# Kernel optimization log

Measured on AMD Instinct MI355X. Metric: run time of the kernel, lower is better.

## Reference

```python
import jax, jax.numpy as jnp
import numpy as np

N_NODES = 50000
N_EDGES = 800000
F_IN = 64
H = 128
N_CLASSES = 10
NUM_GRAPHS = 512


def setup_inputs() -> dict:
    key = jax.random.key(0)
    ks = jax.random.split(key, 16)
    x = jax.random.normal(ks[0], (N_NODES, F_IN), dtype=jnp.float32)
    edge_index = jax.random.randint(ks[1], (2, N_EDGES), 0, N_NODES, dtype=jnp.int64)
    batch = jnp.sort(jax.random.randint(ks[2], (N_NODES,), 0, NUM_GRAPHS, dtype=jnp.int64))

    def lin(k, fi, fo):
        kw, kb = jax.random.split(k)
        s = 1.0 / np.sqrt(fi)
        return (jax.random.uniform(kw, (fi, fo), jnp.float32, -s, s),
                jax.random.uniform(kb, (fo,), jnp.float32, -s, s))

    W0, b0 = lin(ks[3], F_IN, H)
    W1, b1 = lin(ks[4], H, H)
    W2, b2 = lin(ks[5], H, H)
    mW0, mb0 = lin(ks[6], H, H)
    mW1, mb1 = lin(ks[7], H, H)
    mW2, mb2 = lin(ks[8], H, N_CLASSES)
    return {"x": x, "edge_index": edge_index, "batch": batch,
            "W0": W0, "b0": b0, "W1": W1, "b1": b1, "W2": W2, "b2": b2,
            "mW0": mW0, "mb0": mb0, "mW1": mW1, "mb1": mb1, "mW2": mW2, "mb2": mb2}


def reference(x, edge_index, batch, W0, b0, W1, b1, W2, b2, mW0, mb0, mW1, mb1, mW2, mb2):
    N = x.shape[0]
    loop = jnp.arange(N, dtype=edge_index.dtype)
    src = jnp.concatenate([edge_index[0], loop])  # add self-loops (PyG GCNConv)
    dst = jnp.concatenate([edge_index[1], loop])
    deg = jax.ops.segment_sum(jnp.ones_like(src, jnp.float32), dst, num_segments=N)
    dinv = jnp.where(deg > 0, deg ** -0.5, 0.0)
    norm = dinv[src] * dinv[dst]  # [E+N]

    def gcn(h, W, b):
        h = h @ W                                   # [N, H]
        msg = h[src] * norm[:, None]                # gather [E+N, H]
        return jax.ops.segment_sum(msg, dst, num_segments=N) + b

    h = jax.nn.relu(gcn(x, W0, b0))
    h = jax.nn.relu(gcn(h, W1, b1))
    h = jax.nn.relu(gcn(h, W2, b2))
    g = jax.ops.segment_sum(h, batch, num_segments=NUM_GRAPHS)  # global_add_pool
    g = jax.nn.relu(g @ mW0 + mb0)
    g = jax.nn.relu(g @ mW1 + mb1)
    return g @ mW2 + mb2  # [NUM_GRAPHS, N_CLASSES]
```

## Files before the change

kernel.cpp:

```cpp
#include <hip/hip_runtime.h>
#include <hip/hip_bf16.h>
#include <stdint.h>

#define N_NODES   50000
#define N_EDGES   800000
#define F_IN      64
#define HID       128
#define N_CLASSES 10
#define NUM_GRAPHS 512

#define NBUCK 128
#define BW    391
#define S1B   400
#define CHUNK 2000
#define MCNT  (NBUCK * S1B)

typedef unsigned int uint32;
typedef __attribute__((ext_vector_type(8))) short bf16x8;
typedef __attribute__((ext_vector_type(4))) float f32x4;

__device__ __forceinline__ float bl(uint32 w) { return __uint_as_float(w << 16); }
__device__ __forceinline__ float bh(uint32 w) { return __uint_as_float(w & 0xffff0000u); }
__device__ __forceinline__ uint32 packbf(float a, float b) {
    uint32 ua = __float_as_uint(a), ub = __float_as_uint(b);
    ua = (ua + 0x7fffu + ((ua >> 16) & 1u)) >> 16;
    ub = (ub + 0x7fffu + ((ub >> 16) & 1u)) >> 16;
    return ua | (ub << 16);
}
__device__ __forceinline__ unsigned short packbf1(float a) {
    uint32 ua = __float_as_uint(a);
    return (unsigned short)((ua + 0x7fffu + ((ua >> 16) & 1u)) >> 16);
}

__global__ __launch_bounds__(256) void prep_kernel(const float4* __restrict__ x, uint2* __restrict__ xb,
                                                   const float* __restrict__ W0, unsigned short* __restrict__ W0t,
                                                   const float* __restrict__ W1, unsigned short* __restrict__ W1t,
                                                   const float* __restrict__ W2, unsigned short* __restrict__ W2t) {
    int i = blockIdx.x * 256 + threadIdx.x;
    if (i < N_NODES * F_IN / 4) {
        float4 v = x[i];
        xb[i] = make_uint2(packbf(v.x, v.y), packbf(v.z, v.w));
    }
    if (i < 64 * 128) {
        int k = i >> 7, j = i & 127;
        W0t[j * (64 + 8) + k] = packbf1(W0[i]);
    }
    int i2 = i - 64 * 128;
    if (i2 >= 0 && i2 < 128 * 128) {
        int k = i2 >> 7, j = i2 & 127;
        W1t[j * (128 + 8) + k] = packbf1(W1[i2]);
        W2t[j * (128 + 8) + k] = packbf1(W2[i2]);
    }
}

__global__ __launch_bounds__(256) void bhist_kernel(const int* __restrict__ dst,
                                                    int* __restrict__ bcnt, int E) {
    __shared__ int cnt[NBUCK];
    int t = threadIdx.x, blk = blockIdx.x;
    if (t < NBUCK) cnt[t] = 0;
    __syncthreads();
    int base = blk * CHUNK;
    for (int i = t; i < CHUNK; i += 256) {
        int e = base + i;
        if (e < E) atomicAdd(&cnt[(uint32)dst[e] / BW], 1);
    }
    __syncthreads();
    if (t < NBUCK) bcnt[t * S1B + blk] = cnt[t];
}

__global__ __launch_bounds__(256) void scanA_kernel(const int* __restrict__ in,
                                                    int* __restrict__ incl,
                                                    int* __restrict__ bsum, int M) {
    __shared__ int s[256];
    int t = threadIdx.x;
    int i = blockIdx.x * 256 + t;
    int v = (i < M) ? in[i] : 0;
    s[t] = v;
    __syncthreads();
    #pragma unroll
    for (int d = 1; d < 256; d <<= 1) {
        int a = (t >= d) ? s[t - d] : 0;
        __syncthreads();
        s[t] += a;
        __syncthreads();
    }
    if (i < M) incl[i] = s[t];
    if (t == 255) bsum[blockIdx.x] = s[255];
}

__global__ __launch_bounds__(256) void scanB_kernel(int* __restrict__ bsum, int NB) {
    __shared__ int s[256];
    int t = threadIdx.x;
    int v = (t < NB) ? bsum[t] : 0;
    s[t] = v;
    __syncthreads();
    #pragma unroll
    for (int d = 1; d < 256; d <<= 1) {
        int a = (t >= d) ? s[t - d] : 0;
        __syncthreads();
        s[t] += a;
        __syncthreads();
    }
    if (t < NB) bsum[t] = s[t] - v;
}

__global__ __launch_bounds__(256) void bscatter_kernel(const int* __restrict__ src,
                                                       const int* __restrict__ dst,
                                                       const int* __restrict__ incl,
                                                       const int* __restrict__ bsum,
                                                       int2* __restrict__ ebuf, int E) {
    __shared__ int cnt[NBUCK];
    __shared__ int cur[NBUCK];
    int t = threadIdx.x, blk = blockIdx.x;
    if (t < NBUCK) cnt[t] = 0;
    __syncthreads();
    int base = blk * CHUNK;
    for (int i = t; i < CHUNK; i += 256) {
        int e = base + i;
        if (e < E) atomicAdd(&cnt[(uint32)dst[e] / BW], 1);
    }
    __syncthreads();
    if (t < NBUCK) {
        int idx = t * S1B + blk;
        cur[t] = bsum[idx >> 8] + incl[idx] - cnt[t];
    }
    __syncthreads();
    for (int i = t; i < CHUNK; i += 256) {
        int e = base + i;
        if (e < E) {
            int d = dst[e];
            int slot = atomicAdd(&cur[(uint32)d / BW], 1);
            ebuf[slot] = make_int2(src[e], d);
        }
    }
}

__global__ __launch_bounds__(256) void bfinal_kernel(const int2* __restrict__ ebuf,
                                                     const int* __restrict__ bcnt,
                                                     const int* __restrict__ incl,
                                                     const int* __restrict__ bsum,
                                                     int* __restrict__ rowptr,
                                                     float* __restrict__ dinv,
                                                     int2* __restrict__ meta, int E, int N) {
    __shared__ int cnt[392];
    __shared__ int startv[400];
    __shared__ int segt[16];
    int t = threadIdx.x, b = blockIdx.x;

    int bs, be;
    {
        int idx = b * S1B;
        bs = bsum[idx >> 8] + incl[idx] - bcnt[idx];
        if (b + 1 >= NBUCK) be = E;
        else {
            int idx1 = (b + 1) * S1B;
            be = bsum[idx1 >> 8] + incl[idx1] - bcnt[idx1];
        }
    }

    for (int i = t; i < 392; i += 256) cnt[i] = 0;
    __syncthreads();
    for (int i = bs + t; i < be; i += 256) {
        int d = ebuf[i].y;
        atomicAdd(&cnt[d - b * BW], 1);
    }
    __syncthreads();

    if (t < 16) {
        int run = 0;
        #pragma unroll
        for (int k = 0; k < 25; k++) {
            int idx = t * 25 + k;
            int c = (idx < 391) ? cnt[idx] : 0;
            startv[idx] = run;
            run += c;
        }
        segt[t] = run;
    }
    __syncthreads();
    if (t == 0) {
        int run = 0;
        #pragma unroll
        for (int j = 0; j < 16; j++) { int s = segt[j]; segt[j] = run; run += s; }
    }
    __syncthreads();
    for (int l = t; l < 391; l += 256) startv[l] += segt[l / 25] + bs;
    __syncthreads();

    int locN = N - b * BW; if (locN > BW) locN = BW;
    for (int l = t; l < locN; l += 256) {
        int g = b * BW + l;
        rowptr[g + 1] = startv[l] + cnt[l];
        dinv[g] = rsqrtf((float)(cnt[l] + 1));
    }
    if (b == 0 && t == 0) rowptr[0] = 0;
    __syncthreads();

    for (int i = bs + t; i < be; i += 256) {
        int2 sd = ebuf[i];
        int slot = atomicAdd(&startv[sd.y - b * BW], 1);
        meta[slot] = sd;
    }
}

__global__ __launch_bounds__(256) void norm_kernel(int2* __restrict__ meta,
                                                   const float* __restrict__ dinv, int E) {
    int i = blockIdx.x * 256 + threadIdx.x;
    if (i < E) {
        int2 m = meta[i];
        meta[i] = make_int2(m.x, __float_as_int(dinv[m.x] * dinv[m.y]));
    }
}

__global__ __launch_bounds__(256) void spmm128_kernel(const int* __restrict__ rowptr,
                                                      const int2* __restrict__ meta,
                                                      const float* __restrict__ dinv,
                                                      const unsigned short* __restrict__ Hin,
                                                      unsigned short* __restrict__ Hout, int N) {
    int wave = threadIdx.x >> 6;
    int lane = threadIdx.x & 63;
    int node = blockIdx.x * 4 + wave;
    if (node >= N) return;
    int q   = lane >> 4;
    int sub = lane & 15;

    const uint4* Hv = (const uint4*)Hin;
    float di = dinv[node];
    float sn = di * di;

    float acc[8];
    if (q == 0) {
        uint4 s = Hv[(size_t)node * 16 + sub];
        acc[0] = sn * bl(s.x); acc[1] = sn * bh(s.x);
        acc[2] = sn * bl(s.y); acc[3] = sn * bh(s.y);
        acc[4] = sn * bl(s.z); acc[5] = sn * bh(s.z);
        acc[6] = sn * bl(s.w); acc[7] = sn * bh(s.w);
    } else {
        #pragma unroll
        for (int v = 0; v < 8; v++) acc[v] = 0.f;
    }

    int e0 = rowptr[node];
    int e1 = rowptr[node + 1];
    for (int e = e0; e < e1; e += 8) {
        int i0 = e + q;
        int i1 = e + 4 + q;
        int2 m0 = (i0 < e1) ? meta[i0] : make_int2(0, 0);
        int2 m1 = (i1 < e1) ? meta[i1] : make_int2(0, 0);
        float n0 = __int_as_float(m0.y);
        float n1 = __int_as_float(m1.y);
        uint4 r0 = Hv[(size_t)m0.x * 16 + sub];
        uint4 r1 = Hv[(size_t)m1.x * 16 + sub];
        acc[0] = fmaf(n0, bl(r0.x), acc[0]); acc[1] = fmaf(n0, bh(r0.x), acc[1]);
        acc[2] = fmaf(n0, bl(r0.y), acc[2]); acc[3] = fmaf(n0, bh(r0.y), acc[3]);
        acc[4] = fmaf(n0, bl(r0.z), acc[4]); acc[5] = fmaf(n0, bh(r0.z), acc[5]);
        acc[6] = fmaf(n0, bl(r0.w), acc[6]); acc[7] = fmaf(n0, bh(r0.w), acc[7]);
        acc[0] = fmaf(n1, bl(r1.x), acc[0]); acc[1] = fmaf(n1, bh(r1.x), acc[1]);
        acc[2] = fmaf(n1, bl(r1.y), acc[2]); acc[3] = fmaf(n1, bh(r1.y), acc[3]);
        acc[4] = fmaf(n1, bl(r1.z), acc[4]); acc[5] = fmaf(n1, bh(r1.z), acc[5]);
        acc[6] = fmaf(n1, bl(r1.w), acc[6]); acc[7] = fmaf(n1, bh(r1.w), acc[7]);
    }

    #pragma unroll
    for (int v = 0; v < 8; v++) {
        acc[v] += __shfl_xor(acc[v], 16);
        acc[v] += __shfl_xor(acc[v], 32);
    }

    if (q == 0) {
        uint4 o;
        o.x = packbf(acc[0], acc[1]);
        o.y = packbf(acc[2], acc[3]);
        o.z = packbf(acc[4], acc[5]);
        o.w = packbf(acc[6], acc[7]);
        ((uint4*)Hout)[(size_t)node * 16 + sub] = o;
    }
}

__global__ __launch_bounds__(256) void spmm64_kernel(const int* __restrict__ rowptr,
                                                     const int2* __restrict__ meta,
                                                     const float* __restrict__ dinv,
                                                     const unsigned short* __restrict__ Hin,
                                                     unsigned short* __restrict__ Hout, int N) {
    int wave = threadIdx.x >> 6;
    int lane = threadIdx.x & 63;
    int node = blockIdx.x * 4 + wave;
    if (node >= N) return;
    int oct = lane >> 3;
    int sub = lane & 7;

    const uint4* Hv = (const uint4*)Hin;
    float di = dinv[node];
    float sn = di * di;

    float acc[8];
    if (oct == 0) {
        uint4 s = Hv[(size_t)node * 8 + sub];
        acc[0] = sn * bl(s.x); acc[1] = sn * bh(s.x);
        acc[2] = sn * bl(s.y); acc[3] = sn * bh(s.y);
        acc[4] = sn * bl(s.z); acc[5] = sn * bh(s.z);
        acc[6] = sn * bl(s.w); acc[7] = sn * bh(s.w);
    } else {
        #pragma unroll
        for (int v = 0; v < 8; v++) acc[v] = 0.f;
    }

    int e0 = rowptr[node];
    int e1 = rowptr[node + 1];
    for (int e = e0; e < e1; e += 16) {
        int i0 = e + oct;
        int i1 = e + 8 + oct;
        int2 m0 = (i0 < e1) ? meta[i0] : make_int2(0, 0);
        int2 m1 = (i1 < e1) ? meta[i1] : make_int2(0, 0);
        float n0 = __int_as_float(m0.y);
        float n1 = __int_as_float(m1.y);
        uint4 r0 = Hv[(size_t)m0.x * 8 + sub];
        uint4 r1 = Hv[(size_t)m1.x * 8 + sub];
        acc[0] = fmaf(n0, bl(r0.x), acc[0]); acc[1] = fmaf(n0, bh(r0.x), acc[1]);
        acc[2] = fmaf(n0, bl(r0.y), acc[2]); acc[3] = fmaf(n0, bh(r0.y), acc[3]);
        acc[4] = fmaf(n0, bl(r0.z), acc[4]); acc[5] = fmaf(n0, bh(r0.z), acc[5]);
        acc[6] = fmaf(n0, bl(r0.w), acc[6]); acc[7] = fmaf(n0, bh(r0.w), acc[7]);
        acc[0] = fmaf(n1, bl(r1.x), acc[0]); acc[1] = fmaf(n1, bh(r1.x), acc[1]);
        acc[2] = fmaf(n1, bl(r1.y), acc[2]); acc[3] = fmaf(n1, bh(r1.y), acc[3]);
        acc[4] = fmaf(n1, bl(r1.z), acc[4]); acc[5] = fmaf(n1, bh(r1.z), acc[5]);
        acc[6] = fmaf(n1, bl(r1.w), acc[6]); acc[7] = fmaf(n1, bh(r1.w), acc[7]);
    }

    #pragma unroll
    for (int v = 0; v < 8; v++) {
        acc[v] += __shfl_xor(acc[v], 8);
        acc[v] += __shfl_xor(acc[v], 16);
        acc[v] += __shfl_xor(acc[v], 32);
    }

    if (oct == 0) {
        uint4 o;
        o.x = packbf(acc[0], acc[1]);
        o.y = packbf(acc[2], acc[3]);
        o.z = packbf(acc[4], acc[5]);
        o.w = packbf(acc[6], acc[7]);
        ((uint4*)Hout)[(size_t)node * 8 + sub] = o;
    }
}

template <int K>
__global__ __launch_bounds__(256) void gemm_mfma_kernel(const unsigned short* __restrict__ A,
                                                        const unsigned short* __restrict__ Wt,
                                                        const float* __restrict__ bias,
                                                        unsigned short* __restrict__ out,
                                                        int N) {
    constexpr int KP = K + 8;
    __shared__ unsigned short Wl[128 * KP];

    int t = threadIdx.x;
    constexpr int TOT = 128 * KP * 2 / 16;
    #pragma unroll
    for (int i = 0; i < (TOT + 255) / 256; i++) {
        int idx = i * 256 + t;
        if (idx < TOT) ((uint4*)Wl)[idx] = ((const uint4*)Wt)[idx];
    }
    __syncthreads();

    int wave = t >> 6;
    int lane = t & 63;
    int rowBase = blockIdx.x * 128 + wave * 32;
    int r0 = rowBase + (lane & 15);
    int r1 = r0 + 16;
    if (r0 >= N) r0 = N - 1;
    if (r1 >= N) r1 = N - 1;
    int kchunk = lane >> 4;
    int colSub = lane & 15;

    f32x4 acc0[8], acc1[8];
    #pragma unroll
    for (int i = 0; i < 8; i++) { acc0[i] = (f32x4)0.0f; acc1[i] = (f32x4)0.0f; }

    #pragma unroll
    for (int s = 0; s < K / 32; s++) {
        bf16x8 a0 = *(const bf16x8*)(A + (size_t)r0 * K + s * 32 + kchunk * 8);
        bf16x8 a1 = *(const bf16x8*)(A + (size_t)r1 * K + s * 32 + kchunk * 8);
        #pragma unroll
        for (int tl = 0; tl < 8; tl++) {
            bf16x8 b = *(const bf16x8*)(Wl + (tl * 16 + colSub) * KP + s * 32 + kchunk * 8);
            acc0[tl] = __builtin_amdgcn_mfma_f32_16x16x32_bf16(a0, b, acc0[tl], 0, 0, 0);
            acc1[tl] = __builtin_amdgcn_mfma_f32_16x16x32_bf16(a1, b, acc1[tl], 0, 0, 0);
        }
    }

    int rowOff = (lane >> 4) * 4;
    #pragma unroll
    for (int tl = 0; tl < 8; tl++) {
        int col = tl * 16 + colSub;
        float bv = bias[col];
        #pragma unroll
        for (int r = 0; r < 4; r++) {
            int rowA = rowBase + rowOff + r;
            int rowB = rowA + 16;
            if (rowA < N) {
                float v = fmaxf(acc0[tl][r] + bv, 0.f);
                out[(size_t)rowA * 128 + col] = packbf1(v);
            }
            if (rowB < N) {
                float v = fmaxf(acc1[tl][r] + bv, 0.f);
                out[(size_t)rowB * 128 + col] = packbf1(v);
            }
        }
    }
}

__device__ __forceinline__ int lowerb(const int* a, int n, int v) {
    int lo = 0, hi = n;
    while (lo < hi) {
        int m = (lo + hi) >> 1;
        if (a[m] < v) lo = m + 1; else hi = m;
    }
    return lo;
}

__global__ __launch_bounds__(256) void pool_mlp_kernel(const unsigned short* __restrict__ H,
                                                       const int* __restrict__ batch,
                                                       const float* __restrict__ mW0, const float* __restrict__ mb0,
                                                       const float* __restrict__ mW1, const float* __restrict__ mb1,
                                                       const float* __restrict__ mW2, const float* __restrict__ mb2,
                                                       float* __restrict__ out, int N) {
    int b = blockIdx.x;
    int t = threadIdx.x;
    int jw = t & 63;
    int g  = t >> 6;
    int lo = lowerb(batch, N, b);
    int hi = lowerb(batch, N, b + 1);

    const uint32* Hu = (const uint32*)H;
    float f0 = 0.f, f1 = 0.f;
    for (int n = lo + g; n < hi; n += 4) {
        uint32 v = Hu[(size_t)n * 64 + jw];
        f0 += bl(v);
        f1 += bh(v);
    }

    __shared__ float part[4][HID];
    __shared__ float l0[HID];
    __shared__ float l1[HID];
    part[g][jw * 2 + 0] = f0;
    part[g][jw * 2 + 1] = f1;
    __syncthreads();
    if (t < 128) l0[t] = part[0][t] + part[1][t] + part[2][t] + part[3][t];
    __syncthreads();

    if (t < 128) {
        int j = t;
        float a0 = mb0[j], a1 = 0.f, a2 = 0.f, a3 = 0.f;
        #pragma unroll 4
        for (int k = 0; k < HID; k += 4) {
            a0 = fmaf(l0[k + 0], mW0[(k + 0) * HID + j], a0);
            a1 = fmaf(l0[k + 1], mW0[(k + 1) * HID + j], a1);
            a2 = fmaf(l0[k + 2], mW0[(k + 2) * HID + j], a2);
            a3 = fmaf(l0[k + 3], mW0[(k + 3) * HID + j], a3);
        }
        l1[j] = fmaxf((a0 + a1) + (a2 + a3), 0.f);
    }
    __syncthreads();

    float c = 0.f;
    if (t < 128) {
        int j = t;
        float a0 = mb1[j], a1 = 0.f, a2 = 0.f, a3 = 0.f;
        #pragma unroll 4
        for (int k = 0; k < HID; k += 4) {
            a0 = fmaf(l1[k + 0], mW1[(k + 0) * HID + j], a0);
            a1 = fmaf(l1[k + 1], mW1[(k + 1) * HID + j], a1);
            a2 = fmaf(l1[k + 2], mW1[(k + 2) * HID + j], a2);
            a3 = fmaf(l1[k + 3], mW1[(k + 3) * HID + j], a3);
        }
        c = fmaxf((a0 + a1) + (a2 + a3), 0.f);
    }
    __syncthreads();
    if (t < 128) l0[t] = c;
    __syncthreads();

    if (t < N_CLASSES) {
        float a0 = mb2[t], a1 = 0.f, a2 = 0.f, a3 = 0.f;
        #pragma unroll 4
        for (int k = 0; k < HID; k += 4) {
            a0 = fmaf(l0[k + 0], mW2[(k + 0) * N_CLASSES + t], a0);
            a1 = fmaf(l0[k + 1], mW2[(k + 1) * N_CLASSES + t], a1);
            a2 = fmaf(l0[k + 2], mW2[(k + 2) * N_CLASSES + t], a2);
            a3 = fmaf(l0[k + 3], mW2[(k + 3) * N_CLASSES + t], a3);
        }
        out[b * N_CLASSES + t] = (a0 + a1) + (a2 + a3);
    }
}

extern "C" void kernel_launch(void* const* d_in, const int* in_sizes, int n_in,
                              void* d_out, int out_size, void* d_ws, size_t ws_size,
                              hipStream_t stream) {
    const float* x     = (const float*)d_in[0];
    const int*   ei    = (const int*)d_in[1];
    const int*   batch = (const int*)d_in[2];
    const float* W0  = (const float*)d_in[3];
    const float* b0  = (const float*)d_in[4];
    const float* W1  = (const float*)d_in[5];
    const float* b1  = (const float*)d_in[6];
    const float* W2  = (const float*)d_in[7];
    const float* b2  = (const float*)d_in[8];
    const float* mW0 = (const float*)d_in[9];
    const float* mb0 = (const float*)d_in[10];
    const float* mW1 = (const float*)d_in[11];
    const float* mb1 = (const float*)d_in[12];
    const float* mW2 = (const float*)d_in[13];
    const float* mb2 = (const float*)d_in[14];
    float* out = (float*)d_out;

    const int N = N_NODES, E = N_EDGES;
    const int* src = ei;
    const int* dst = ei + E;

    char* w = (char*)d_ws;
    auto alloc = [&](size_t bytes) -> void* {
        void* p = (void*)w;
        w += (bytes + 255) & ~(size_t)255;
        return p;
    };
    int*   rowptr = (int*)alloc((size_t)(N + 1) * 4);
    int2*  ebuf   = (int2*)alloc((size_t)E * 8);
    int2*  meta   = (int2*)alloc((size_t)E * 8);
    int*   bcnt   = (int*)alloc((size_t)MCNT * 4);
    int*   incl   = (int*)alloc((size_t)MCNT * 4);
    int*   bsum   = (int*)alloc(256 * 4);
    float* dinv   = (float*)alloc((size_t)N * 4);
    unsigned short* xb   = (unsigned short*)alloc((size_t)N * F_IN * 2);
    unsigned short* bufA = (unsigned short*)alloc((size_t)N * HID * 2);
    unsigned short* bufB = (unsigned short*)alloc((size_t)N * HID * 2);
    unsigned short* W0t  = (unsigned short*)alloc((size_t)128 * (64 + 8) * 2);
    unsigned short* W1t  = (unsigned short*)alloc((size_t)128 * (128 + 8) * 2);
    unsigned short* W2t  = (unsigned short*)alloc((size_t)128 * (128 + 8) * 2);

    const int EB  = (E + 255) / 256;
    const int SPB = (N + 3) / 4;
    const int GB  = (N + 127) / 128;
    const int PB  = (N * F_IN / 4 + 255) / 256;
    const int SCB = (MCNT + 255) / 256;

    prep_kernel<<<PB, 256, 0, stream>>>((const float4*)x, (uint2*)xb,
                                        W0, W0t, W1, W1t, W2, W2t);
    bhist_kernel<<<S1B, 256, 0, stream>>>(dst, bcnt, E);
    scanA_kernel<<<SCB, 256, 0, stream>>>(bcnt, incl, bsum, MCNT);
    scanB_kernel<<<1, 256, 0, stream>>>(bsum, SCB);
    bscatter_kernel<<<S1B, 256, 0, stream>>>(src, dst, incl, bsum, ebuf, E);
    bfinal_kernel<<<NBUCK, 256, 0, stream>>>(ebuf, bcnt, incl, bsum, rowptr, dinv, meta, E, N);
    norm_kernel<<<EB, 256, 0, stream>>>(meta, dinv, E);

    spmm64_kernel<<<SPB, 256, 0, stream>>>(rowptr, meta, dinv, xb, bufA, N);
    gemm_mfma_kernel<64><<<GB, 256, 0, stream>>>(bufA, W0t, b0, bufB, N);

    spmm128_kernel<<<SPB, 256, 0, stream>>>(rowptr, meta, dinv, bufB, bufA, N);
    gemm_mfma_kernel<128><<<GB, 256, 0, stream>>>(bufA, W1t, b1, bufB, N);

    spmm128_kernel<<<SPB, 256, 0, stream>>>(rowptr, meta, dinv, bufB, bufA, N);
    gemm_mfma_kernel<128><<<GB, 256, 0, stream>>>(bufA, W2t, b2, bufB, N);

    pool_mlp_kernel<<<NUM_GRAPHS, 256, 0, stream>>>(bufB, batch, mW0, mb0, mW1, mb1, mW2, mb2, out, N);
}
```

Before: 219.9 us.

## Slice SpMM feature columns across blocks so each wave processes 32 edges per step

Replaces the per-node SpMM kernels with one templated kernel. Each block now handles a 64-byte column slice of the feature row, and the wave spreads 16 edge lanes × 2 across neighbours instead of 4 or 8. This gives more memory-level parallelism per wave for average degree 16 and launches 2–4× more blocks. In exchange, each slice re-reads rowptr and meta, gathers only 64-byte segments per neighbour row, and the reduction takes four shuffle steps instead of two.

```diff
diff --git a/kernel.cpp b/kernel.cpp
--- a/kernel.cpp
+++ b/kernel.cpp
@@ -212,45 +212,48 @@
     }
 }
 
-__global__ __launch_bounds__(256) void spmm128_kernel(const int* __restrict__ rowptr,
-                                                      const int2* __restrict__ meta,
-                                                      const float* __restrict__ dinv,
-                                                      const unsigned short* __restrict__ Hin,
-                                                      unsigned short* __restrict__ Hout, int N) {
-    int wave = threadIdx.x >> 6;
-    int lane = threadIdx.x & 63;
-    int node = blockIdx.x * 4 + wave;
+template <int RC>
+__global__ __launch_bounds__(256) void spmm_sliced_kernel(const int* __restrict__ rowptr,
+                                                          const int2* __restrict__ meta,
+                                                          const float* __restrict__ dinv,
+                                                          const unsigned short* __restrict__ Hin,
+                                                          unsigned short* __restrict__ Hout, int N) {
+    constexpr int NPS = (N_NODES + 3) / 4;
+    int slice = blockIdx.x / NPS;
+    int bis   = blockIdx.x - slice * NPS;
+    int wave  = threadIdx.x >> 6;
+    int lane  = threadIdx.x & 63;
+    int node  = bis * 4 + wave;
     if (node >= N) return;
-    int q   = lane >> 4;
-    int sub = lane & 15;
+    int q   = lane & 15;
+    int sub = (lane >> 4) + slice * 4;
 
     const uint4* Hv = (const uint4*)Hin;
     float di = dinv[node];
     float sn = di * di;
 
     float acc[8];
+    #pragma unroll
+    for (int v = 0; v < 8; v++) acc[v] = 0.f;
     if (q == 0) {
-        uint4 s = Hv[(size_t)node * 16 + sub];
+        uint4 s = Hv[(size_t)node * RC + sub];
         acc[0] = sn * bl(s.x); acc[1] = sn * bh(s.x);
         acc[2] = sn * bl(s.y); acc[3] = sn * bh(s.y);
         acc[4] = sn * bl(s.z); acc[5] = sn * bh(s.z);
         acc[6] = sn * bl(s.w); acc[7] = sn * bh(s.w);
-    } else {
-        #pragma unroll
-        for (int v = 0; v < 8; v++) acc[v] = 0.f;
     }
 
     int e0 = rowptr[node];
     int e1 = rowptr[node + 1];
-    for (int e = e0; e < e1; e += 8) {
+    for (int e = e0; e < e1; e += 32) {
         int i0 = e + q;
-        int i1 = e + 4 + q;
+        int i1 = e + 16 + q;
         int2 m0 = (i0 < e1) ? meta[i0] : make_int2(0, 0);
         int2 m1 = (i1 < e1) ? meta[i1] : make_int2(0, 0);
         float n0 = __int_as_float(m0.y);
         float n1 = __int_as_float(m1.y);
-        uint4 r0 = Hv[(size_t)m0.x * 16 + sub];
-        uint4 r1 = Hv[(size_t)m1.x * 16 + sub];
+        uint4 r0 = Hv[(size_t)m0.x * RC + sub];
+        uint4 r1 = Hv[(size_t)m1.x * RC + sub];
         acc[0] = fmaf(n0, bl(r0.x), acc[0]); acc[1] = fmaf(n0, bh(r0.x), acc[1]);
         acc[2] = fmaf(n0, bl(r0.y), acc[2]); acc[3] = fmaf(n0, bh(r0.y), acc[3]);
         acc[4] = fmaf(n0, bl(r0.z), acc[4]); acc[5] = fmaf(n0, bh(r0.z), acc[5]);
@@ -263,8 +266,10 @@
 
     #pragma unroll
     for (int v = 0; v < 8; v++) {
-        acc[v] += __shfl_xor(acc[v], 16);
-        acc[v] += __shfl_xor(acc[v], 32);
+        acc[v] += __shfl_xor(acc[v], 1);
+        acc[v] += __shfl_xor(acc[v], 2);
+        acc[v] += __shfl_xor(acc[v], 4);
+        acc[v] += __shfl_xor(acc[v], 8);
     }
 
     if (q == 0) {
@@ -273,73 +278,7 @@
         o.y = packbf(acc[2], acc[3]);
         o.z = packbf(acc[4], acc[5]);
         o.w = packbf(acc[6], acc[7]);
-        ((uint4*)Hout)[(size_t)node * 16 + sub] = o;
-    }
-}
-
-__global__ __launch_bounds__(256) void spmm64_kernel(const int* __restrict__ rowptr,
-                                                     const int2* __restrict__ meta,
-                                                     const float* __restrict__ dinv,
-                                                     const unsigned short* __restrict__ Hin,
-                                                     unsigned short* __restrict__ Hout, int N) {
-    int wave = threadIdx.x >> 6;
-    int lane = threadIdx.x & 63;
-    int node = blockIdx.x * 4 + wave;
-    if (node >= N) return;
-    int oct = lane >> 3;
-    int sub = lane & 7;
-
-    const uint4* Hv = (const uint4*)Hin;
-    float di = dinv[node];
-    float sn = di * di;
-
-    float acc[8];
-    if (oct == 0) {
-        uint4 s = Hv[(size_t)node * 8 + sub];
-        acc[0] = sn * bl(s.x); acc[1] = sn * bh(s.x);
-        acc[2] = sn * bl(s.y); acc[3] = sn * bh(s.y);
-        acc[4] = sn * bl(s.z); acc[5] = sn * bh(s.z);
-        acc[6] = sn * bl(s.w); acc[7] = sn * bh(s.w);
-    } else {
-        #pragma unroll
-        for (int v = 0; v < 8; v++) acc[v] = 0.f;
-    }
-
-    int e0 = rowptr[node];
-    int e1 = rowptr[node + 1];
-    for (int e = e0; e < e1; e += 16) {
-        int i0 = e + oct;
-        int i1 = e + 8 + oct;
-        int2 m0 = (i0 < e1) ? meta[i0] : make_int2(0, 0);
-        int2 m1 = (i1 < e1) ? meta[i1] : make_int2(0, 0);
-        float n0 = __int_as_float(m0.y);
-        float n1 = __int_as_float(m1.y);
-        uint4 r0 = Hv[(size_t)m0.x * 8 + sub];
-        uint4 r1 = Hv[(size_t)m1.x * 8 + sub];
-        acc[0] = fmaf(n0, bl(r0.x), acc[0]); acc[1] = fmaf(n0, bh(r0.x), acc[1]);
-        acc[2] = fmaf(n0, bl(r0.y), acc[2]); acc[3] = fmaf(n0, bh(r0.y), acc[3]);
-        acc[4] = fmaf(n0, bl(r0.z), acc[4]); acc[5] = fmaf(n0, bh(r0.z), acc[5]);
-        acc[6] = fmaf(n0, bl(r0.w), acc[6]); acc[7] = fmaf(n0, bh(r0.w), acc[7]);
-        acc[0] = fmaf(n1, bl(r1.x), acc[0]); acc[1] = fmaf(n1, bh(r1.x), acc[1]);
-        acc[2] = fmaf(n1, bl(r1.y), acc[2]); acc[3] = fmaf(n1, bh(r1.y), acc[3]);
-        acc[4] = fmaf(n1, bl(r1.z), acc[4]); acc[5] = fmaf(n1, bh(r1.z), acc[5]);
-        acc[6] = fmaf(n1, bl(r1.w), acc[6]); acc[7] = fmaf(n1, bh(r1.w), acc[7]);
-    }
-
-    #pragma unroll
-    for (int v = 0; v < 8; v++) {
-        acc[v] += __shfl_xor(acc[v], 8);
-        acc[v] += __shfl_xor(acc[v], 16);
-        acc[v] += __shfl_xor(acc[v], 32);
-    }
-
-    if (oct == 0) {
-        uint4 o;
-        o.x = packbf(acc[0], acc[1]);
-        o.y = packbf(acc[2], acc[3]);
-        o.z = packbf(acc[4], acc[5]);
-        o.w = packbf(acc[6], acc[7]);
-        ((uint4*)Hout)[(size_t)node * 8 + sub] = o;
+        ((uint4*)Hout)[(size_t)node * RC + sub] = o;
     }
 }
 
@@ -535,11 +474,11 @@
     unsigned short* W1t  = (unsigned short*)alloc((size_t)128 * (128 + 8) * 2);
     unsigned short* W2t  = (unsigned short*)alloc((size_t)128 * (128 + 8) * 2);
 
-    const int EB  = (E + 255) / 256;
-    const int SPB = (N + 3) / 4;
-    const int GB  = (N + 127) / 128;
-    const int PB  = (N * F_IN / 4 + 255) / 256;
-    const int SCB = (MCNT + 255) / 256;
+    const int EB   = (E + 255) / 256;
+    const int NPS  = (N + 3) / 4;
+    const int GB   = (N + 127) / 128;
+    const int PB   = (N * F_IN / 4 + 255) / 256;
+    const int SCB  = (MCNT + 255) / 256;
 
     prep_kernel<<<PB, 256, 0, stream>>>((const float4*)x, (uint2*)xb,
                                         W0, W0t, W1, W1t, W2, W2t);
@@ -550,13 +489,13 @@
     bfinal_kernel<<<NBUCK, 256, 0, stream>>>(ebuf, bcnt, incl, bsum, rowptr, dinv, meta, E, N);
     norm_kernel<<<EB, 256, 0, stream>>>(meta, dinv, E);
 
-    spmm64_kernel<<<SPB, 256, 0, stream>>>(rowptr, meta, dinv, xb, bufA, N);
+    spmm_sliced_kernel<8><<<NPS * 2, 256, 0, stream>>>(rowptr, meta, dinv, xb, bufA, N);
     gemm_mfma_kernel<64><<<GB, 256, 0, stream>>>(bufA, W0t, b0, bufB, N);
 
-    spmm128_kernel<<<SPB, 256, 0, stream>>>(rowptr, meta, dinv, bufB, bufA, N);
+    spmm_sliced_kernel<16><<<NPS * 4, 256, 0, stream>>>(rowptr, meta, dinv, bufB, bufA, N);
     gemm_mfma_kernel<128><<<GB, 256, 0, stream>>>(bufA, W1t, b1, bufB, N);
 
-    spmm128_kernel<<<SPB, 256, 0, stream>>>(rowptr, meta, dinv, bufB, bufA, N);
+    spmm_sliced_kernel<16><<<NPS * 4, 256, 0, stream>>>(rowptr, meta, dinv, bufB, bufA, N);
     gemm_mfma_kernel<128><<<GB, 256, 0, stream>>>(bufA, W2t, b2, bufB, N);
 
     pool_mlp_kernel<<<NUM_GRAPHS, 256, 0, stream>>>(bufB, batch, mW0, mb0, mW1, mb1, mW2, mb2, out, N);
```

New measurement: 318.4 us. 1.45x slower.
